# Kernel optimization log

Measured on AMD Instinct MI355X. Metric: run time of the kernel, lower is better.

## Reference

```python
import jax, jax.numpy as jnp
import numpy as np

N_NODES = 50000
N_EDGES = 600000
DIM = 128
N_REL = 3
LN_EPS = 1e-5


def setup_inputs() -> dict:
    key = jax.random.key(0)
    ks = jax.random.split(key, 8)
    x = jax.random.normal(ks[0], (N_NODES, DIM), dtype=jnp.float32)
    edge_index = jax.random.randint(ks[1], (2, N_EDGES), 0, N_NODES, dtype=jnp.int64)
    edge_type = jax.random.randint(ks[2], (N_EDGES,), 0, N_REL, dtype=jnp.int64)
    # learned params
    relation_weights = jax.random.normal(ks[3], (N_REL, DIM, DIM), dtype=jnp.float32)
    lim = 1.0 / np.sqrt(DIM)
    lin_w = jax.random.uniform(ks[4], (DIM, DIM), dtype=jnp.float32, minval=-lim, maxval=lim)
    lin_b = jax.random.uniform(ks[5], (DIM,), dtype=jnp.float32, minval=-lim, maxval=lim)
    ln_gamma = jnp.ones((DIM,), dtype=jnp.float32)
    ln_beta = jnp.zeros((DIM,), dtype=jnp.float32)
    return {"x": x, "edge_index": edge_index, "edge_type": edge_type,
            "relation_weights": relation_weights, "lin_w": lin_w, "lin_b": lin_b,
            "ln_gamma": ln_gamma, "ln_beta": ln_beta}


def reference(x, edge_index, edge_type, relation_weights, lin_w, lin_b, ln_gamma, ln_beta):
    # x: [N, D]; edge_index: [2, E]; edge_type: [E]
    N = x.shape[0]
    src, dst = edge_index[0], edge_index[1]
    xs = x[src]  # gather: [E, D]
    # relation-wise masked GEMM accumulated into per-edge messages
    msg = jnp.zeros_like(xs)
    for r in range(relation_weights.shape[0]):  # small fixed relation loop
        mask = (edge_type == r)[:, None]
        msg = msg + jnp.where(mask, xs @ relation_weights[r], jnp.zeros((), x.dtype))
    agg = jax.ops.segment_sum(msg, dst, num_segments=N)  # scatter-add: [N, D]
    deg = jax.ops.segment_sum(jnp.ones_like(dst, dtype=x.dtype), dst, num_segments=N)
    deg = jnp.maximum(deg, 1.0)
    out = agg / deg[:, None]
    # linear + residual + LayerNorm (eps 1e-5, biased variance)
    h = x @ lin_w.T + lin_b + out
    mu = jnp.mean(h, axis=-1, keepdims=True)
    var = jnp.mean((h - mu) ** 2, axis=-1, keepdims=True)
    return ln_gamma * (h - mu) * jax.lax.rsqrt(var + LN_EPS) + ln_beta
```

## Files before the change

### kernel.cpp

```cpp
#include <hip/hip_runtime.h>

#define DIM    128
#define NREL   3
#define KS     (NREL*DIM)
#define NB     16
#define LN_EPS 1e-5f
#define PPART  32
#define KSLOT  24
#define PW     (PPART*KSLOT)
#define OVFP   512
#define CH     256
#define GPREP  1024

typedef unsigned int uint;
typedef unsigned char uchar;
typedef float f32x4 __attribute__((ext_vector_type(4)));
typedef short short8 __attribute__((ext_vector_type(8)));

__device__ __forceinline__ unsigned short f2bf(float f) {
    union { float f; uint u; } c; c.f = f;
    return (unsigned short)((c.u + 0x7fffu + ((c.u >> 16) & 1u)) >> 16);
}
__device__ __forceinline__ uint packbf(float a, float b) {
    return (uint)f2bf(a) | ((uint)f2bf(b) << 16);
}
__device__ __forceinline__ float blo(uint u) {
    union { uint u; float f; } c; c.u = u << 16; return c.f;
}
__device__ __forceinline__ float bhi(uint u) {
    union { uint u; float f; } c; c.u = u & 0xffff0000u; return c.f;
}
__device__ __forceinline__ int ldidx(const int* p, size_t i, int i64) {
    return i64 ? p[2*i] : p[i];
}
__device__ __forceinline__ int fo(int m, int k) {
    return ((k >> 5) << 6) + ((((k >> 3) & 3)) << 4) + m;
}
__device__ __forceinline__ int SW(int s) { return s ^ ((s >> 4) & 7); }

__device__ __forceinline__ void block_probe(const int* __restrict__ ei, int t, int* s_i64) {
    if (t < 64) {
        int z = 0;
        #pragma unroll
        for (int i = 0; i < 4; i++) z += (ei[t*4 + i] == 0) ? 1 : 0;
        #pragma unroll
        for (int off = 1; off < 64; off <<= 1) z += __shfl_xor(z, off);
        if (t == 0) *s_i64 = (z > 64) ? 1 : 0;
    }
}

__device__ __forceinline__ void bpack_work(int idx, const float* __restrict__ relw,
                                           const float* __restrict__ linw,
                                           unsigned short* __restrict__ Bpack) {
    if (idx < 8192) {
        int lane = idx & 63, kk = (idx >> 6) & 15, tile = idx >> 10;
        int q = lane >> 4, n = tile * 16 + (lane & 15);
        uint vv[4];
        #pragma unroll
        for (int jp = 0; jp < 4; jp++) {
            int k0 = kk * 32 + q * 8 + jp * 2;
            float v0 = (k0     < KS) ? relw[(size_t)k0*DIM + n]
                                     : linw[(size_t)n*DIM + (k0 - KS)];
            float v1 = (k0 + 1 < KS) ? relw[(size_t)(k0+1)*DIM + n]
                                     : linw[(size_t)n*DIM + (k0 + 1 - KS)];
            vv[jp] = packbf(v0, v1);
        }
        uint4 v; v.x = vv[0]; v.y = vv[1]; v.z = vv[2]; v.w = vv[3];
        ((uint4*)Bpack)[idx] = v;
    }
}

__global__ __launch_bounds__(1024)
void prep_kernel(const int* __restrict__ ei, const int* __restrict__ et,
                 const float* __restrict__ x, int E, int N, int Ee, int NBIN,
                 uchar* __restrict__ cnt, int* __restrict__ binbuf,
                 int* __restrict__ ovf_cnt, int2* __restrict__ ovf,
                 const float* __restrict__ relw, const float* __restrict__ linw,
                 unsigned short* __restrict__ Bpack, unsigned short* __restrict__ xbf)
{
    extern __shared__ int lhist[];
    __shared__ int s_i64;
    __shared__ int s_ovf;
    const int b = blockIdx.x, t = threadIdx.x;

    if (b < PPART) {
        block_probe(ei, t, &s_i64);
        if (t == 0) s_ovf = 0;
        for (int i = t; i < NBIN; i += 1024) lhist[i] = 0;
        __syncthreads();
        const int i64 = s_i64;
        const int e0 = b * Ee;
        const int e1 = min(E, e0 + Ee);
        for (int e = e0 + t; e < e1; e += 1024) {
            int s = ldidx(ei, (size_t)e, i64);
            int d = ldidx(ei, (size_t)E + e, i64);
            int r = ldidx(et, (size_t)e, i64);
            int bin = d >> 4;
            int tag = s | ((d & 15) << 20) | (r << 24);
            int lr = atomicAdd(&lhist[bin], 1);
            if (lr < KSLOT) {
                binbuf[bin * PW + b * KSLOT + lr] = tag;
            } else {
                int oi = atomicAdd(&s_ovf, 1);
                if (oi < OVFP) ovf[b * OVFP + oi] = make_int2(tag, bin);
            }
        }
        __syncthreads();
        for (int i = t; i < NBIN; i += 1024)
            cnt[i * PPART + b] = (uchar)min(lhist[i], KSLOT);
        if (t == 0) ovf_cnt[b] = min(s_ovf, OVFP);
    } else {
        const int cid  = (b - PPART) * 1024 + t;
        const int nthr = (GPREP - PPART) * 1024;
        const float4* x4 = (const float4*)x;
        const int items = N * (DIM / 8);
        for (int i = cid; i < items; i += nthr) {
            float4 a = x4[i*2], bb = x4[i*2 + 1];
            uint4 v;
            v.x = packbf(a.x, a.y); v.y = packbf(a.z, a.w);
            v.z = packbf(bb.x, bb.y); v.w = packbf(bb.z, bb.w);
            ((uint4*)xbf)[i] = v;
        }
        bpack_work(cid, relw, linw, Bpack);
    }
}

__global__ __launch_bounds__(256)
void main_kernel(const unsigned short* __restrict__ xbf,
                 const uchar* __restrict__ cnt,
                 const int* __restrict__ binbuf,
                 const int* __restrict__ ovf_cnt, const int2* __restrict__ ovf,
                 const unsigned short* __restrict__ Bpack,
                 const float* __restrict__ linb,
                 const float* __restrict__ gamma,
                 const float* __restrict__ beta,
                 float* __restrict__ out, int N)
{
    __shared__ uint4 Af[1024];
    __shared__ int s_cnt[48];
    __shared__ int s_off[49];
    __shared__ int s_cur[48];
    __shared__ int s_coff[PPART + 1];
    __shared__ int s_n;
    __shared__ int s_ovfL;
    __shared__ float s_mu[NB], s_rs[NB];

    int* s_tag = (int*)Af;
    int* s_cmp = (int*)Af + 256;
    int* s_map = (int*)Af + 512;

    const int t  = threadIdx.x;
    const int bb = blockIdx.x;
    const int n0 = bb * NB;
    const int m  = t >> 4;
    const int c  = t & 15;
    const int n  = n0 + m;

    const uint4* xh = (const uint4*)xbf;

    float a0[8], a1[8], a2[8];
    #pragma unroll
    for (int i = 0; i < 8; i++) { a0[i] = 0.f; a1[i] = 0.f; a2[i] = 0.f; }
    int deg = 0;
    uint4 res = {0,0,0,0};
    if (n < N) res = xh[(size_t)n*16 + c];

    if (t < 64) {
        int cv = (t < PPART) ? (int)cnt[(size_t)bb * PPART + t] : 0;
        int v = cv;
        #pragma unroll
        for (int off = 1; off < PPART; off <<= 1) {
            int u = __shfl_up(v, off);
            if (t >= off) v += u;
        }
        if (t < PPART) s_coff[t + 1] = v;
        if (t == 0) s_coff[0] = 0;
    }
    if (t >= 64 && t < 128) {
        int lv = (t - 64 < PPART) ? ovf_cnt[t - 64] : 0;
        #pragma unroll
        for (int off = 1; off < 64; off <<= 1) lv += __shfl_xor(lv, off);
        if (t == 64) s_ovfL = lv;
    }
    __syncthreads();

    #define FINISH_CHUNK(NC) { \
        const int nc_ = (NC); \
        if (t < 64) { \
            int cv_ = (t < 48) ? s_cnt[t] : 0; \
            int v_ = cv_; \
            _Pragma("unroll") \
            for (int off = 1; off < 64; off <<= 1) { \
                int u_ = __shfl_up(v_, off); \
                if (t >= off) v_ += u_; \
            } \
            if (t < 48) { s_off[t + 1] = v_; s_cur[t] = v_ - cv_; } \
            if (t == 0) s_off[0] = 0; \
        } \
        __syncthreads(); \
        if (t < nc_) { \
            int pos_ = atomicAdd(&s_cur[key], 1); \
            s_cmp[pos_] = tg & 0xFFFFF; \
        } \
        __syncthreads(); \
        deg += s_off[m*3 + 3] - s_off[m*3]; \
        { \
            int p_ = s_off[m*3 + 0], pe_ = s_off[m*3 + 1]; \
            GATH(a0) \
            p_ = s_off[m*3 + 1]; pe_ = s_off[m*3 + 2]; \
            GATH(a1) \
            p_ = s_off[m*3 + 2]; pe_ = s_off[m*3 + 3]; \
            GATH(a2) \
        } \
        __syncthreads(); }

    #define GATH(ACC) \
        for (; p_ + 3 < pe_; p_ += 4) { \
            int s0 = s_cmp[p_],   s1 = s_cmp[p_+1]; \
            int s2 = s_cmp[p_+2], s3 = s_cmp[p_+3]; \
            uint4 g0 = xh[(size_t)s0*16 + c], g1 = xh[(size_t)s1*16 + c]; \
            uint4 g2 = xh[(size_t)s2*16 + c], g3 = xh[(size_t)s3*16 + c]; \
            ACC[0] += blo(g0.x)+blo(g1.x)+blo(g2.x)+blo(g3.x); \
            ACC[1] += bhi(g0.x)+bhi(g1.x)+bhi(g2.x)+bhi(g3.x); \
            ACC[2] += blo(g0.y)+blo(g1.y)+blo(g2.y)+blo(g3.y); \
            ACC[3] += bhi(g0.y)+bhi(g1.y)+bhi(g2.y)+bhi(g3.y); \
            ACC[4] += blo(g0.z)+blo(g1.z)+blo(g2.z)+blo(g3.z); \
            ACC[5] += bhi(g0.z)+bhi(g1.z)+bhi(g2.z)+bhi(g3.z); \
            ACC[6] += blo(g0.w)+blo(g1.w)+blo(g2.w)+blo(g3.w); \
            ACC[7] += bhi(g0.w)+bhi(g1.w)+bhi(g2.w)+bhi(g3.w); \
        } \
        for (; p_ < pe_; ++p_) { \
            int s0 = s_cmp[p_]; \
            uint4 g0 = xh[(size_t)s0*16 + c]; \
            ACC[0] += blo(g0.x); ACC[1] += bhi(g0.x); \
            ACC[2] += blo(g0.y); ACC[3] += bhi(g0.y); \
            ACC[4] += blo(g0.z); ACC[5] += bhi(g0.z); \
            ACC[6] += blo(g0.w); ACC[7] += bhi(g0.w); \
        }

    int g0 = 0;
    while (g0 < PPART) {
        const int base0 = s_coff[g0];
        int gend = g0;
        while (gend < PPART && s_coff[gend + 1] - base0 <= CH) ++gend;
        const int nc = s_coff[gend] - base0;
        if (t < 48) s_cnt[t] = 0;
        for (int cell = g0 + t; cell < gend; cell += 256) {
            int lo = s_coff[cell] - base0, hi = s_coff[cell + 1] - base0;
            for (int s2 = lo; s2 < hi; ++s2) s_map[s2] = cell;
        }
        __syncthreads();
        int key = -1, tg = 0;
        if (t < nc) {
            int cell = s_map[t];
            int slot = t - (s_coff[cell] - base0);
            tg = binbuf[(size_t)bb * PW + cell * KSLOT + slot];
            key = (((tg >> 20) & 15) * 3) + ((tg >> 24) & 3);
            atomicAdd(&s_cnt[key], 1);
        }
        __syncthreads();
        FINISH_CHUNK(nc)
        g0 = gend;
    }

    if (s_ovfL > 0) {
        if (t == 0) s_n = 0;
        if (t < 48) s_cnt[t] = 0;
        __syncthreads();
        for (int p = 0; p < PPART; p++) {
            int L = ovf_cnt[p];
            for (int i = t; i < L; i += 256) {
                int2 o = ovf[p * OVFP + i];
                if (o.y == bb) {
                    int pos = atomicAdd(&s_n, 1);
                    if (pos < CH) s_tag[pos] = o.x;
                }
            }
        }
        __syncthreads();
        int nc = min(s_n, CH);
        int key = -1, tg = 0;
        if (t < nc) {
            tg = s_tag[t];
            key = (((tg >> 20) & 15) * 3) + ((tg >> 24) & 3);
            atomicAdd(&s_cnt[key], 1);
        }
        __syncthreads();
        FINISH_CHUNK(nc)
    }
    #undef GATH
    #undef FINISH_CHUNK

    {
        float inv = 1.0f / fmaxf((float)deg, 1.0f);
        uint4 w0;
        w0.x = packbf(a0[0]*inv, a0[1]*inv); w0.y = packbf(a0[2]*inv, a0[3]*inv);
        w0.z = packbf(a0[4]*inv, a0[5]*inv); w0.w = packbf(a0[6]*inv, a0[7]*inv);
        Af[SW(fo(m, 0*DIM + 8*c))] = w0;
        w0.x = packbf(a1[0]*inv, a1[1]*inv); w0.y = packbf(a1[2]*inv, a1[3]*inv);
        w0.z = packbf(a1[4]*inv, a1[5]*inv); w0.w = packbf(a1[6]*inv, a1[7]*inv);
        Af[SW(fo(m, 1*DIM + 8*c))] = w0;
        w0.x = packbf(a2[0]*inv, a2[1]*inv); w0.y = packbf(a2[2]*inv, a2[3]*inv);
        w0.z = packbf(a2[4]*inv, a2[5]*inv); w0.w = packbf(a2[6]*inv, a2[7]*inv);
        Af[SW(fo(m, 2*DIM + 8*c))] = w0;
        Af[SW(fo(m, KS + 8*c))] = res;
    }
    __syncthreads();

    const int lane = t & 63;
    const int w    = t >> 6;
    const int mm   = lane & 15;
    const int q    = lane >> 4;
    f32x4 acc0 = {0,0,0,0}, acc1 = {0,0,0,0};
    {
        const short8* Aq = (const short8*)Af;
        const short8* Bq = (const short8*)Bpack;
        #pragma unroll
        for (int kk = 0; kk < 16; kk++) {
            short8 a  = Aq[SW(kk*64 + lane)];
            short8 b0 = Bq[((w*2 + 0)*16 + kk)*64 + lane];
            short8 b1 = Bq[((w*2 + 1)*16 + kk)*64 + lane];
            acc0 = __builtin_amdgcn_mfma_f32_16x16x32_bf16(a, b0, acc0, 0, 0, 0);
            acc1 = __builtin_amdgcn_mfma_f32_16x16x32_bf16(a, b1, acc1, 0, 0, 0);
        }
    }
    __syncthreads();

    float* H = (float*)Af;
    {
        int rb = q * 4;
        #pragma unroll
        for (int nt = 0; nt < 2; nt++) {
            int d = (w*2 + nt)*16 + mm;
            float lb = linb[d];
            f32x4 a = (nt == 0) ? acc0 : acc1;
            #pragma unroll
            for (int i = 0; i < 4; i++)
                H[(rb + i)*132 + d] = a[i] + lb;
        }
    }
    __syncthreads();

    {
        int j = t >> 4, p = t & 15;
        float s1 = 0.f, s2 = 0.f;
        const float* hr = &H[j*132 + p*8];
        #pragma unroll
        for (int i = 0; i < 8; i++) { float v = hr[i]; s1 += v; s2 += v*v; }
        #pragma unroll
        for (int off = 1; off < 16; off <<= 1) {
            s1 += __shfl_xor(s1, off);
            s2 += __shfl_xor(s2, off);
        }
        if (p == 0) {
            float mu  = s1 * (1.0f/DIM);
            float var = s2 * (1.0f/DIM) - mu*mu;
            s_mu[j] = mu;
            s_rs[j] = rsqrtf(var + LN_EPS);
        }
    }
    __syncthreads();

    {
        int d  = t & 127;
        int jb = (t >> 7) * 8;
        float g = gamma[d];
        float b = beta[d];
        #pragma unroll
        for (int jj = 0; jj < 8; jj++) {
            int j = jb + jj;
            int nn = n0 + j;
            if (nn < N) {
                float hv = H[j*132 + d];
                out[(size_t)nn*DIM + d] = g * (hv - s_mu[j]) * s_rs[j] + b;
            }
        }
    }
}

extern "C" void kernel_launch(void* const* d_in, const int* in_sizes, int n_in,
                              void* d_out, int out_size, void* d_ws, size_t ws_size,
                              hipStream_t stream)
{
    const float* x   = (const float*)d_in[0];
    const int*   ei  = (const int*)d_in[1];
    const int*   et  = (const int*)d_in[2];
    const float* rw  = (const float*)d_in[3];
    const float* lw  = (const float*)d_in[4];
    const float* lb  = (const float*)d_in[5];
    const float* lg  = (const float*)d_in[6];
    const float* lbe = (const float*)d_in[7];

    const int N    = in_sizes[0] / DIM;
    const int E    = in_sizes[2];
    const int NBIN = (N + NB - 1) / NB;
    const int Ee   = (E + PPART - 1) / PPART;

    char* wp = (char*)d_ws;
    int*  ovf_cnt = (int*)wp;             wp += 128;
    int2* ovf     = (int2*)wp;            wp += (size_t)PPART * OVFP * 8;
    uchar* cnt    = (uchar*)wp;           wp += ((size_t)NBIN * PPART + 63) & ~(size_t)63;
    int*  binbuf  = (int*)wp;             wp += (size_t)NBIN * PW * 4;
    unsigned short* Bpack = (unsigned short*)wp;   wp += 512 * 128 * 2;
    unsigned short* xbf   = (unsigned short*)wp;   wp += (size_t)N * DIM * 2;
    (void)ws_size;

    prep_kernel<<<GPREP, 1024, (size_t)NBIN * 4, stream>>>(ei, et, x, E, N, Ee, NBIN,
                                                           cnt, binbuf, ovf_cnt, ovf,
                                                           rw, lw, Bpack, xbf);
    main_kernel<<<NBIN, 256, 0, stream>>>(xbf, cnt, binbuf, ovf_cnt, ovf, Bpack,
                                          lb, lg, lbe, (float*)d_out, N);
}
```

Baseline: 188.0 us.

## Split prep into edge-binning and conversion kernels with more edge partitions

The combined prep kernel is split into a separate edge-binning kernel and an x/weight bf16 conversion kernel. Edge partitions grow from 32 to 128 blocks, each with fewer slots per bin, so the binning phase runs on more CUs. The main kernel's prefix scan now handles 128 partition counts across waves, and a fast path skips the chunk-boundary search when all cells fit in one chunk. The cost is an extra kernel launch, more cnt bytes per bin for the main kernel to scan, and smaller overflow buffers that could overflow more often.

Result: slower. 306.6 us (+63.1%).

```diff
diff --git a/kernel.cpp b/kernel.cpp
--- a/kernel.cpp
+++ b/kernel.cpp
@@ -5,12 +5,11 @@
 #define KS     (NREL*DIM)
 #define NB     16
 #define LN_EPS 1e-5f
-#define PPART  32
-#define KSLOT  24
+#define PPART  128
+#define KSLOT  6
 #define PW     (PPART*KSLOT)
-#define OVFP   512
+#define OVFP   64
 #define CH     256
-#define GPREP  1024
 
 typedef unsigned int uint;
 typedef unsigned char uchar;
@@ -70,59 +69,61 @@
     }
 }
 
-__global__ __launch_bounds__(1024)
-void prep_kernel(const int* __restrict__ ei, const int* __restrict__ et,
-                 const float* __restrict__ x, int E, int N, int Ee, int NBIN,
+__global__ __launch_bounds__(512)
+void edge_kernel(const int* __restrict__ ei, const int* __restrict__ et,
+                 int E, int Ee, int NBIN,
                  uchar* __restrict__ cnt, int* __restrict__ binbuf,
-                 int* __restrict__ ovf_cnt, int2* __restrict__ ovf,
-                 const float* __restrict__ relw, const float* __restrict__ linw,
-                 unsigned short* __restrict__ Bpack, unsigned short* __restrict__ xbf)
+                 int* __restrict__ ovf_cnt, int2* __restrict__ ovf)
 {
     extern __shared__ int lhist[];
     __shared__ int s_i64;
     __shared__ int s_ovf;
     const int b = blockIdx.x, t = threadIdx.x;
 
-    if (b < PPART) {
-        block_probe(ei, t, &s_i64);
-        if (t == 0) s_ovf = 0;
-        for (int i = t; i < NBIN; i += 1024) lhist[i] = 0;
-        __syncthreads();
-        const int i64 = s_i64;
-        const int e0 = b * Ee;
-        const int e1 = min(E, e0 + Ee);
-        for (int e = e0 + t; e < e1; e += 1024) {
-            int s = ldidx(ei, (size_t)e, i64);
-            int d = ldidx(ei, (size_t)E + e, i64);
-            int r = ldidx(et, (size_t)e, i64);
-            int bin = d >> 4;
-            int tag = s | ((d & 15) << 20) | (r << 24);
-            int lr = atomicAdd(&lhist[bin], 1);
-            if (lr < KSLOT) {
-                binbuf[bin * PW + b * KSLOT + lr] = tag;
-            } else {
-                int oi = atomicAdd(&s_ovf, 1);
-                if (oi < OVFP) ovf[b * OVFP + oi] = make_int2(tag, bin);
-            }
-        }
-        __syncthreads();
-        for (int i = t; i < NBIN; i += 1024)
-            cnt[i * PPART + b] = (uchar)min(lhist[i], KSLOT);
-        if (t == 0) ovf_cnt[b] = min(s_ovf, OVFP);
-    } else {
-        const int cid  = (b - PPART) * 1024 + t;
-        const int nthr = (GPREP - PPART) * 1024;
-        const float4* x4 = (const float4*)x;
-        const int items = N * (DIM / 8);
-        for (int i = cid; i < items; i += nthr) {
-            float4 a = x4[i*2], bb = x4[i*2 + 1];
-            uint4 v;
-            v.x = packbf(a.x, a.y); v.y = packbf(a.z, a.w);
-            v.z = packbf(bb.x, bb.y); v.w = packbf(bb.z, bb.w);
-            ((uint4*)xbf)[i] = v;
-        }
-        bpack_work(cid, relw, linw, Bpack);
-    }
+    block_probe(ei, t, &s_i64);
+    if (t == 0) s_ovf = 0;
+    for (int i = t; i < NBIN; i += 512) lhist[i] = 0;
+    __syncthreads();
+    const int i64 = s_i64;
+    const int e0 = b * Ee;
+    const int e1 = min(E, e0 + Ee);
+    for (int e = e0 + t; e < e1; e += 512) {
+        int s = ldidx(ei, (size_t)e, i64);
+        int d = ldidx(ei, (size_t)E + e, i64);
+        int r = ldidx(et, (size_t)e, i64);
+        int bin = d >> 4;
+        int tag = s | ((d & 15) << 20) | (r << 24);
+        int lr = atomicAdd(&lhist[bin], 1);
+        if (lr < KSLOT) {
+            binbuf[bin * PW + b * KSLOT + lr] = tag;
+        } else {
+            int oi = atomicAdd(&s_ovf, 1);
+            if (oi < OVFP) ovf[b * OVFP + oi] = make_int2(tag, bin);
+        }
+    }
+    __syncthreads();
+    for (int i = t; i < NBIN; i += 512)
+        cnt[i * PPART + b] = (uchar)min(lhist[i], KSLOT);
+    if (t == 0) ovf_cnt[b] = min(s_ovf, OVFP);
+}
+
+__global__ __launch_bounds__(256)
+void convert_kernel(const float* __restrict__ x, int N,
+                    const float* __restrict__ relw, const float* __restrict__ linw,
+                    unsigned short* __restrict__ Bpack, unsigned short* __restrict__ xbf)
+{
+    const int tid  = blockIdx.x * 256 + threadIdx.x;
+    const int nthr = gridDim.x * 256;
+    const float4* x4 = (const float4*)x;
+    const int items = N * (DIM / 8);
+    for (int i = tid; i < items; i += nthr) {
+        float4 a = x4[i*2], bb = x4[i*2 + 1];
+        uint4 v;
+        v.x = packbf(a.x, a.y); v.y = packbf(a.z, a.w);
+        v.z = packbf(bb.x, bb.y); v.w = packbf(bb.z, bb.w);
+        ((uint4*)xbf)[i] = v;
+    }
+    bpack_work(tid, relw, linw, Bpack);
 }
 
 __global__ __launch_bounds__(256)
@@ -141,6 +142,7 @@
     __shared__ int s_off[49];
     __shared__ int s_cur[48];
     __shared__ int s_coff[PPART + 1];
+    __shared__ int s_ws[4];
     __shared__ int s_n;
     __shared__ int s_ovfL;
     __shared__ float s_mu[NB], s_rs[NB];
@@ -155,6 +157,8 @@
     const int m  = t >> 4;
     const int c  = t & 15;
     const int n  = n0 + m;
+    const int lane = t & 63;
+    const int wv   = t >> 6;
 
     const uint4* xh = (const uint4*)xbf;
 
@@ -165,22 +169,30 @@
     uint4 res = {0,0,0,0};
     if (n < N) res = xh[(size_t)n*16 + c];
 
-    if (t < 64) {
-        int cv = (t < PPART) ? (int)cnt[(size_t)bb * PPART + t] : 0;
-        int v = cv;
-        #pragma unroll
-        for (int off = 1; off < PPART; off <<= 1) {
-            int u = __shfl_up(v, off);
-            if (t >= off) v += u;
-        }
-        if (t < PPART) s_coff[t + 1] = v;
-        if (t == 0) s_coff[0] = 0;
-    }
-    if (t >= 64 && t < 128) {
-        int lv = (t - 64 < PPART) ? ovf_cnt[t - 64] : 0;
-        #pragma unroll
-        for (int off = 1; off < 64; off <<= 1) lv += __shfl_xor(lv, off);
-        if (t == 64) s_ovfL = lv;
+    if (t == 0) s_ovfL = 0;
+    int vsc = 0;
+    if (t < PPART) vsc = (int)cnt[(size_t)bb * PPART + t];
+    {
+        #pragma unroll
+        for (int off = 1; off < 64; off <<= 1) {
+            int u = __shfl_up(vsc, off);
+            if (lane >= off) vsc += u;
+        }
+        if (t < PPART && lane == 63) s_ws[wv] = vsc;
+    }
+    __syncthreads();
+    if (t < PPART) {
+        int wpre = 0;
+        #pragma unroll
+        for (int k = 0; k < (PPART/64) - 1; k++) if (k < wv) wpre += s_ws[k];
+        s_coff[t + 1] = vsc + wpre;
+    }
+    if (t == 0) s_coff[0] = 0;
+    {
+        int ov = (t < PPART) ? ovf_cnt[t] : 0;
+        #pragma unroll
+        for (int off = 1; off < 64; off <<= 1) ov += __shfl_xor(ov, off);
+        if (lane == 0 && t < PPART) atomicAdd(&s_ovfL, ov);
     }
     __syncthreads();
 
@@ -241,8 +253,13 @@
     int g0 = 0;
     while (g0 < PPART) {
         const int base0 = s_coff[g0];
-        int gend = g0;
-        while (gend < PPART && s_coff[gend + 1] - base0 <= CH) ++gend;
+        int gend;
+        if (s_coff[PPART] - base0 <= CH) {
+            gend = PPART;
+        } else {
+            gend = g0;
+            while (gend < PPART && s_coff[gend + 1] - base0 <= CH) ++gend;
+        }
         const int nc = s_coff[gend] - base0;
         if (t < 48) s_cnt[t] = 0;
         for (int cell = g0 + t; cell < gend; cell += 256) {
@@ -307,8 +324,7 @@
     }
     __syncthreads();
 
-    const int lane = t & 63;
-    const int w    = t >> 6;
+    const int w    = wv;
     const int mm   = lane & 15;
     const int q    = lane >> 4;
     f32x4 acc0 = {0,0,0,0}, acc1 = {0,0,0,0};
@@ -397,7 +413,7 @@
     const int Ee   = (E + PPART - 1) / PPART;
 
     char* wp = (char*)d_ws;
-    int*  ovf_cnt = (int*)wp;             wp += 128;
+    int*  ovf_cnt = (int*)wp;             wp += 512;
     int2* ovf     = (int2*)wp;            wp += (size_t)PPART * OVFP * 8;
     uchar* cnt    = (uchar*)wp;           wp += ((size_t)NBIN * PPART + 63) & ~(size_t)63;
     int*  binbuf  = (int*)wp;             wp += (size_t)NBIN * PW * 4;
@@ -405,9 +421,10 @@
     unsigned short* xbf   = (unsigned short*)wp;   wp += (size_t)N * DIM * 2;
     (void)ws_size;
 
-    prep_kernel<<<GPREP, 1024, (size_t)NBIN * 4, stream>>>(ei, et, x, E, N, Ee, NBIN,
-                                                           cnt, binbuf, ovf_cnt, ovf,
-                                                           rw, lw, Bpack, xbf);
+    edge_kernel<<<PPART, 512, (size_t)NBIN * 4, stream>>>(ei, et, E, Ee, NBIN,
+                                                          cnt, binbuf, ovf_cnt, ovf);
+    convert_kernel<<<(N * (DIM/8) + 255) / 256, 256, 0, stream>>>(x, N, rw, lw,
+                                                                  Bpack, xbf);
     main_kernel<<<NBIN, 256, 0, stream>>>(xbf, cnt, binbuf, ovf_cnt, ovf, Bpack,
                                           lb, lg, lbe, (float*)d_out, N);
 }
```
